# Optimization experiments

Hardware: AMD Instinct MI355X
Metric: run time of the kernel (lower is better)

## Reference

```python
import jax, jax.numpy as jnp
import numpy as np

N_NODES = 100000
N_EDGES = 1600000
IN_C, HID_C, OUT_C = 128, 128, 64


def setup_inputs() -> dict:
    key = jax.random.key(0)
    ks = jax.random.split(key, 8)
    x = jax.random.normal(ks[0], (N_NODES, IN_C), dtype=jnp.float32)
    edge_index = jax.random.randint(ks[1], (2, N_EDGES), 0, N_NODES, dtype=jnp.int64)
    # SAGEConv params: lin_l (aggregated neighbors, with bias), lin_r (root, no bias)
    s1 = 1.0 / np.sqrt(IN_C)
    s2 = 1.0 / np.sqrt(HID_C)
    W1_l = jax.random.uniform(ks[2], (IN_C, HID_C), jnp.float32, -s1, s1)
    b1_l = jnp.zeros((HID_C,), jnp.float32)
    W1_r = jax.random.uniform(ks[3], (IN_C, HID_C), jnp.float32, -s1, s1)
    W2_l = jax.random.uniform(ks[4], (HID_C, OUT_C), jnp.float32, -s2, s2)
    b2_l = jnp.zeros((OUT_C,), jnp.float32)
    W2_r = jax.random.uniform(ks[5], (HID_C, OUT_C), jnp.float32, -s2, s2)
    return {"x": x, "edge_index": edge_index, "W1_l": W1_l, "b1_l": b1_l,
            "W1_r": W1_r, "W2_l": W2_l, "b2_l": b2_l, "W2_r": W2_r}


def _sage_conv(x, src, dst, W_l, b_l, W_r):
    # gather source features, scatter-max reduce onto destinations
    msg = x[src]                                             # [E, C]
    aggr = jax.ops.segment_max(msg, dst, num_segments=N_NODES)
    aggr = jnp.where(jnp.isfinite(aggr), aggr, 0.0)          # isolated nodes -> 0 (PyG behavior)
    return aggr @ W_l + b_l + x @ W_r


def reference(x, edge_index, W1_l, b1_l, W1_r, W2_l, b2_l, W2_r):
    src, dst = edge_index[0], edge_index[1]
    h = _sage_conv(x, src, dst, W1_l, b1_l, W1_r)
    h = jax.nn.relu(h)
    # dropout is identity in eval mode
    out = _sage_conv(h, src, dst, W2_l, b2_l, W2_r)
    return out
```

## Files before the change

### kernel.cpp

```cpp
#include <hip/hip_runtime.h>
#include <cstdint>

#define NNODES 100000
#define NEDGES 1600000
#define NBKT   196
#define CAP    9216
#define BIN_CHUNK 4096
#define GBIN ((NEDGES + BIN_CHUNK - 1) / BIN_CHUNK)
#define GCVT (NNODES * 128 / 8 / 256)

typedef __attribute__((ext_vector_type(8))) __bf16 bf16x8;
typedef __attribute__((ext_vector_type(4))) float f32x4;
typedef short v2s __attribute__((ext_vector_type(2)));

__device__ __forceinline__ unsigned short f2bf_rne(float f) {
    unsigned int u = __float_as_uint(f);
    u += 0x7fffu + ((u >> 16) & 1u);
    return (unsigned short)(u >> 16);
}
__device__ __forceinline__ unsigned encdec(unsigned u) {
    return u ^ (((u & 0x80008000u) >> 15) * 0x7FFFu);
}
__device__ __forceinline__ unsigned pkmax(unsigned a, unsigned b) {
    v2s r = __builtin_elementwise_max(__builtin_bit_cast(v2s, a), __builtin_bit_cast(v2s, b));
    return __builtin_bit_cast(unsigned, r);
}

__global__ __launch_bounds__(256) void prep1_kernel(
        const float* __restrict__ W1l, const float* __restrict__ W1r,
        const float* __restrict__ W2l, const float* __restrict__ W2r,
        uint4* __restrict__ Wf1, uint4* __restrict__ Wf2,
        int* __restrict__ bucketFill) {
    if (blockIdx.x == 24) { bucketFill[threadIdx.x] = 0; return; }
    int t = blockIdx.x * 256 + threadIdx.x;
    unsigned short s[8];
    if (t < 4096) {
        int h = t >> 11, kt = (t >> 9) & 3, nt = (t >> 6) & 7, lane = t & 63;
        const float* W = h ? W1r : W1l;
        int k0 = kt * 32 + (lane >> 4) * 8;
        int col = nt * 16 + (lane & 15);
#pragma unroll
        for (int j = 0; j < 8; ++j) s[j] = f2bf_rne(W[(k0 + j) * 128 + col]);
        uint4 o;
        o.x = (unsigned)s[0] | ((unsigned)s[1] << 16);
        o.y = (unsigned)s[2] | ((unsigned)s[3] << 16);
        o.z = (unsigned)s[4] | ((unsigned)s[5] << 16);
        o.w = (unsigned)s[6] | ((unsigned)s[7] << 16);
        Wf1[t] = o;
    } else {
        int u = t - 4096;
        int h = u >> 10, kt = (u >> 8) & 3, nt = (u >> 6) & 3, lane = u & 63;
        const float* W = h ? W2r : W2l;
        int k0 = kt * 32 + (lane >> 4) * 8;
        int col = nt * 16 + (lane & 15);
#pragma unroll
        for (int j = 0; j < 8; ++j) s[j] = f2bf_rne(W[(k0 + j) * 64 + col]);
        uint4 o;
        o.x = (unsigned)s[0] | ((unsigned)s[1] << 16);
        o.y = (unsigned)s[2] | ((unsigned)s[3] << 16);
        o.z = (unsigned)s[4] | ((unsigned)s[5] << 16);
        o.w = (unsigned)s[6] | ((unsigned)s[7] << 16);
        Wf2[u] = o;
    }
}

__global__ __launch_bounds__(256) void prep2_kernel(
        const int* __restrict__ src, const int* __restrict__ dst,
        unsigned int* __restrict__ binArr, int* __restrict__ bucketFill,
        const float4* __restrict__ xin, uint4* __restrict__ xeout, int nE) {
    if (blockIdx.x >= GBIN) {
        int i = (blockIdx.x - GBIN) * 256 + threadIdx.x;
        float4 v0 = xin[(size_t)2 * i], v1 = xin[(size_t)2 * i + 1];
        uint4 o;
        o.x = encdec((unsigned)f2bf_rne(v0.x) | ((unsigned)f2bf_rne(v0.y) << 16));
        o.y = encdec((unsigned)f2bf_rne(v0.z) | ((unsigned)f2bf_rne(v0.w) << 16));
        o.z = encdec((unsigned)f2bf_rne(v1.x) | ((unsigned)f2bf_rne(v1.y) << 16));
        o.w = encdec((unsigned)f2bf_rne(v1.z) | ((unsigned)f2bf_rne(v1.w) << 16));
        xeout[i] = o;
        return;
    }
    __shared__ unsigned int stage[BIN_CHUNK];
    __shared__ unsigned char bof[BIN_CHUNK];
    __shared__ int cnt[256], cstart[256], cfill[256], gbase[256];
    const int tid = threadIdx.x;
    const int blockStart = blockIdx.x * BIN_CHUNK;
    const int chunkN = min(BIN_CHUNK, nE - blockStart);
    cnt[tid] = 0;
    __syncthreads();
    int myd[16], mys[16];
#pragma unroll
    for (int i = 0; i < 16; ++i) {
        int idx = i * 256 + tid;
        if (idx < chunkN) {
            myd[i] = dst[blockStart + idx];
            mys[i] = src[blockStart + idx];
            atomicAdd(&cnt[myd[i] >> 9], 1);
        }
    }
    __syncthreads();
    int v = cnt[tid];
    for (int off = 1; off < 256; off <<= 1) {
        int add = (tid >= off) ? cnt[tid - off] : 0;
        __syncthreads();
        cnt[tid] += add;
        __syncthreads();
    }
    cstart[tid] = cnt[tid] - v;
    cfill[tid] = cnt[tid] - v;
    if (tid < NBKT && v > 0) gbase[tid] = atomicAdd(&bucketFill[tid], v);
    __syncthreads();
#pragma unroll
    for (int i = 0; i < 16; ++i) {
        int idx = i * 256 + tid;
        if (idx < chunkN) {
            int b = myd[i] >> 9;
            int p = atomicAdd(&cfill[b], 1);
            stage[p] = ((unsigned)(myd[i] & 511) << 17) | (unsigned)mys[i];
            bof[p] = (unsigned char)b;
        }
    }
    __syncthreads();
#pragma unroll
    for (int i = 0; i < 16; ++i) {
        int idx = i * 256 + tid;
        if (idx < chunkN) {
            int b = bof[idx];
            int slot = gbase[b] + (idx - cstart[b]);
            if (slot < CAP) binArr[(size_t)b * CAP + slot] = stage[idx];
        }
    }
}

__global__ __launch_bounds__(512) void build_csr_kernel(
        const unsigned int* __restrict__ binArr, const int* __restrict__ bucketFill,
        unsigned int* __restrict__ sortedSrc,
        int* __restrict__ rowBeg, int* __restrict__ rowEnd) {
    __shared__ unsigned int stage[CAP];
    __shared__ int ncnt[512], nstart[512];
    const int b = blockIdx.x;
    const int t = threadIdx.x;
    const int cnt_b = min(bucketFill[b], CAP);
    ncnt[t] = 0;
    __syncthreads();
    for (int i = t; i < cnt_b; i += 512) {
        unsigned int e = binArr[(size_t)b * CAP + i];
        stage[i] = e;
        atomicAdd(&ncnt[e >> 17], 1);
    }
    __syncthreads();
    int v = ncnt[t];
    for (int off = 1; off < 512; off <<= 1) {
        int add = (t >= off) ? ncnt[t - off] : 0;
        __syncthreads();
        ncnt[t] += add;
        __syncthreads();
    }
    int start = ncnt[t] - v;
    nstart[t] = start;
    int n = (b << 9) + t;
    if (n < NNODES) {
        rowBeg[n] = b * CAP + start;
        rowEnd[n] = b * CAP + start + v;
    }
    __syncthreads();
    for (int i = t; i < cnt_b; i += 512) {
        unsigned int e = stage[i];
        int p = atomicAdd(&nstart[e >> 17], 1);
        sortedSrc[(size_t)b * CAP + p] = e & 0x1FFFFu;
    }
}

__global__ __launch_bounds__(256) void aggregate_pk2(
        const uint4* __restrict__ xe4,
        const int* __restrict__ rowBeg,
        const int* __restrict__ rowEnd,
        const unsigned int* __restrict__ sortedSrc,
        uint4* __restrict__ aggrE,
        int nN) {
    const int wv = threadIdx.x >> 6;
    const int lane = threadIdx.x & 63;
    const int grp = lane >> 4;
    const int nA = blockIdx.x * 8 + wv * 2;
    const int nB = nA + 1;
    if (nA >= nN) return;
    const int begA = rowBeg[nA], endA = rowEnd[nA];
    int begB = 0, endB = 0;
    if (nB < nN) { begB = rowBeg[nB]; endB = rowEnd[nB]; }
    const int mA = endA - begA, mB = endB - begB;

    int idA = (mA > 0) ? (int)sortedSrc[min(begA + lane, endA - 1)] : 0;
    int idB = (mB > 0) ? (int)sortedSrc[min(begB + lane, endB - 1)] : 0;

    unsigned aA0 = 0x80008000u, aA1 = 0x80008000u, aA2 = 0x80008000u, aA3 = 0x80008000u;
    unsigned aB0 = 0x80008000u, aB1 = 0x80008000u, aB2 = 0x80008000u, aB3 = 0x80008000u;

    const int cA = min(mA, 64), cB = min(mB, 64);
    const int mm = max(cA, cB);
    for (int j = 0; j < mm; j += 16) {
        const bool doA = j < cA, doB = j < cB;
        uint4 pA0, pA1, pA2, pA3, pB0, pB1, pB2, pB3;
        if (doA) {
            int s0 = __shfl(idA, j + grp);
            int s1 = __shfl(idA, j + 4 + grp);
            int s2 = __shfl(idA, j + 8 + grp);
            int s3 = __shfl(idA, j + 12 + grp);
            pA0 = xe4[(size_t)s0 * 16 + (lane & 15)];
            pA1 = xe4[(size_t)s1 * 16 + (lane & 15)];
            pA2 = xe4[(size_t)s2 * 16 + (lane & 15)];
            pA3 = xe4[(size_t)s3 * 16 + (lane & 15)];
        }
        if (doB) {
            int s0 = __shfl(idB, j + grp);
            int s1 = __shfl(idB, j + 4 + grp);
            int s2 = __shfl(idB, j + 8 + grp);
            int s3 = __shfl(idB, j + 12 + grp);
            pB0 = xe4[(size_t)s0 * 16 + (lane & 15)];
            pB1 = xe4[(size_t)s1 * 16 + (lane & 15)];
            pB2 = xe4[(size_t)s2 * 16 + (lane & 15)];
            pB3 = xe4[(size_t)s3 * 16 + (lane & 15)];
        }
        if (doA) {
            aA0 = pkmax(aA0, pkmax(pkmax(pA0.x, pA1.x), pkmax(pA2.x, pA3.x)));
            aA1 = pkmax(aA1, pkmax(pkmax(pA0.y, pA1.y), pkmax(pA2.y, pA3.y)));
            aA2 = pkmax(aA2, pkmax(pkmax(pA0.z, pA1.z), pkmax(pA2.z, pA3.z)));
            aA3 = pkmax(aA3, pkmax(pkmax(pA0.w, pA1.w), pkmax(pA2.w, pA3.w)));
        }
        if (doB) {
            aB0 = pkmax(aB0, pkmax(pkmax(pB0.x, pB1.x), pkmax(pB2.x, pB3.x)));
            aB1 = pkmax(aB1, pkmax(pkmax(pB0.y, pB1.y), pkmax(pB2.y, pB3.y)));
            aB2 = pkmax(aB2, pkmax(pkmax(pB0.z, pB1.z), pkmax(pB2.z, pB3.z)));
            aB3 = pkmax(aB3, pkmax(pkmax(pB0.w, pB1.w), pkmax(pB2.w, pB3.w)));
        }
    }
    for (int bs = begA + 64; bs < endA; bs += 64) {
        int bid = (int)sortedSrc[min(bs + lane, endA - 1)];
        const int m = min(endA - bs, 64);
        for (int j = 0; j < m; j += 16) {
            int s0 = __shfl(bid, j + grp);
            int s1 = __shfl(bid, j + 4 + grp);
            int s2 = __shfl(bid, j + 8 + grp);
            int s3 = __shfl(bid, j + 12 + grp);
            uint4 p0 = xe4[(size_t)s0 * 16 + (lane & 15)];
            uint4 p1 = xe4[(size_t)s1 * 16 + (lane & 15)];
            uint4 p2 = xe4[(size_t)s2 * 16 + (lane & 15)];
            uint4 p3 = xe4[(size_t)s3 * 16 + (lane & 15)];
            aA0 = pkmax(aA0, pkmax(pkmax(p0.x, p1.x), pkmax(p2.x, p3.x)));
            aA1 = pkmax(aA1, pkmax(pkmax(p0.y, p1.y), pkmax(p2.y, p3.y)));
            aA2 = pkmax(aA2, pkmax(pkmax(p0.z, p1.z), pkmax(p2.z, p3.z)));
            aA3 = pkmax(aA3, pkmax(pkmax(p0.w, p1.w), pkmax(p2.w, p3.w)));
        }
    }
    for (int bs = begB + 64; bs < endB; bs += 64) {
        int bid = (int)sortedSrc[min(bs + lane, endB - 1)];
        const int m = min(endB - bs, 64);
        for (int j = 0; j < m; j += 16) {
            int s0 = __shfl(bid, j + grp);
            int s1 = __shfl(bid, j + 4 + grp);
            int s2 = __shfl(bid, j + 8 + grp);
            int s3 = __shfl(bid, j + 12 + grp);
            uint4 p0 = xe4[(size_t)s0 * 16 + (lane & 15)];
            uint4 p1 = xe4[(size_t)s1 * 16 + (lane & 15)];
            uint4 p2 = xe4[(size_t)s2 * 16 + (lane & 15)];
            uint4 p3 = xe4[(size_t)s3 * 16 + (lane & 15)];
            aB0 = pkmax(aB0, pkmax(pkmax(p0.x, p1.x), pkmax(p2.x, p3.x)));
            aB1 = pkmax(aB1, pkmax(pkmax(p0.y, p1.y), pkmax(p2.y, p3.y)));
            aB2 = pkmax(aB2, pkmax(pkmax(p0.z, p1.z), pkmax(p2.z, p3.z)));
            aB3 = pkmax(aB3, pkmax(pkmax(p0.w, p1.w), pkmax(p2.w, p3.w)));
        }
    }
    aA0 = pkmax(aA0, (unsigned)__shfl_xor((int)aA0, 16));
    aA1 = pkmax(aA1, (unsigned)__shfl_xor((int)aA1, 16));
    aA2 = pkmax(aA2, (unsigned)__shfl_xor((int)aA2, 16));
    aA3 = pkmax(aA3, (unsigned)__shfl_xor((int)aA3, 16));
    aB0 = pkmax(aB0, (unsigned)__shfl_xor((int)aB0, 16));
    aB1 = pkmax(aB1, (unsigned)__shfl_xor((int)aB1, 16));
    aB2 = pkmax(aB2, (unsigned)__shfl_xor((int)aB2, 16));
    aB3 = pkmax(aB3, (unsigned)__shfl_xor((int)aB3, 16));
    aA0 = pkmax(aA0, (unsigned)__shfl_xor((int)aA0, 32));
    aA1 = pkmax(aA1, (unsigned)__shfl_xor((int)aA1, 32));
    aA2 = pkmax(aA2, (unsigned)__shfl_xor((int)aA2, 32));
    aA3 = pkmax(aA3, (unsigned)__shfl_xor((int)aA3, 32));
    aB0 = pkmax(aB0, (unsigned)__shfl_xor((int)aB0, 32));
    aB1 = pkmax(aB1, (unsigned)__shfl_xor((int)aB1, 32));
    aB2 = pkmax(aB2, (unsigned)__shfl_xor((int)aB2, 32));
    aB3 = pkmax(aB3, (unsigned)__shfl_xor((int)aB3, 32));
    if (lane < 16) {
        uint4 o;
        if (mA > 0) { o.x = aA0; o.y = aA1; o.z = aA2; o.w = aA3; }
        else        { o.x = o.y = o.z = o.w = 0u; }
        aggrE[(size_t)nA * 16 + lane] = o;
    } else if (lane < 32 && nB < nN) {
        uint4 o;
        if (mB > 0) { o.x = aB0; o.y = aB1; o.z = aB2; o.w = aB3; }
        else        { o.x = o.y = o.z = o.w = 0u; }
        aggrE[(size_t)nB * 16 + (lane - 16)] = o;
    }
}

template<int BN, bool RELU, bool ENCOUT, typename OutT>
__global__ __launch_bounds__(256, 4) void sage_gemm_lean(
        const uint4* __restrict__ AggE,
        const uint4* __restrict__ RootE,
        const uint4* __restrict__ Wf,
        const float* __restrict__ bias,
        OutT* __restrict__ C,
        int M) {
    constexpr int NT = BN / 16;
    const int tid = threadIdx.x;
    const int w = tid >> 6;
    const int lane = tid & 63;
    const int quad = lane >> 4;
    const int mrow = lane & 15;
    const int base0 = blockIdx.x * 128 + w * 32;

    const int r0 = min(base0 + mrow, M - 1);
    const int r1 = min(base0 + 16 + mrow, M - 1);

    f32x4 acc[2][NT];
#pragma unroll
    for (int mt = 0; mt < 2; ++mt)
#pragma unroll
        for (int nt = 0; nt < NT; ++nt) acc[mt][nt] = (f32x4){0.f, 0.f, 0.f, 0.f};

#pragma unroll
    for (int kt = 0; kt < 4; ++kt) {
        uint4 ta0 = AggE[(size_t)r0 * 16 + kt * 4 + quad];
        uint4 ta1 = AggE[(size_t)r1 * 16 + kt * 4 + quad];
        uint4 tr0 = RootE[(size_t)r0 * 16 + kt * 4 + quad];
        uint4 tr1 = RootE[(size_t)r1 * 16 + kt * 4 + quad];
        ta0.x = encdec(ta0.x); ta0.y = encdec(ta0.y); ta0.z = encdec(ta0.z); ta0.w = encdec(ta0.w);
        ta1.x = encdec(ta1.x); ta1.y = encdec(ta1.y); ta1.z = encdec(ta1.z); ta1.w = encdec(ta1.w);
        tr0.x = encdec(tr0.x); tr0.y = encdec(tr0.y); tr0.z = encdec(tr0.z); tr0.w = encdec(tr0.w);
        tr1.x = encdec(tr1.x); tr1.y = encdec(tr1.y); tr1.z = encdec(tr1.z); tr1.w = encdec(tr1.w);
        bf16x8 aa0 = __builtin_bit_cast(bf16x8, ta0);
        bf16x8 aa1 = __builtin_bit_cast(bf16x8, ta1);
        bf16x8 ar0 = __builtin_bit_cast(bf16x8, tr0);
        bf16x8 ar1 = __builtin_bit_cast(bf16x8, tr1);
#pragma unroll
        for (int nt = 0; nt < NT; ++nt) {
            bf16x8 b0 = __builtin_bit_cast(bf16x8, Wf[(kt * NT + nt) * 64 + lane]);
            acc[0][nt] = __builtin_amdgcn_mfma_f32_16x16x32_bf16(aa0, b0, acc[0][nt], 0, 0, 0);
            acc[1][nt] = __builtin_amdgcn_mfma_f32_16x16x32_bf16(aa1, b0, acc[1][nt], 0, 0, 0);
            bf16x8 b1 = __builtin_bit_cast(bf16x8, Wf[((4 + kt) * NT + nt) * 64 + lane]);
            acc[0][nt] = __builtin_amdgcn_mfma_f32_16x16x32_bf16(ar0, b1, acc[0][nt], 0, 0, 0);
            acc[1][nt] = __builtin_amdgcn_mfma_f32_16x16x32_bf16(ar1, b1, acc[1][nt], 0, 0, 0);
        }
    }

#pragma unroll
    for (int mt = 0; mt < 2; ++mt) {
        const int rowD = base0 + mt * 16 + quad * 4;
#pragma unroll
        for (int nt = 0; nt < NT; ++nt) {
            int col = nt * 16 + mrow;
            float bv = bias[col];
#pragma unroll
            for (int r = 0; r < 4; ++r) {
                int grow = rowD + r;
                if (grow < M) {
                    float v = acc[mt][nt][r] + bv;
                    if (RELU) v = fmaxf(v, 0.0f);
                    if constexpr (ENCOUT) {
                        unsigned u = f2bf_rne(v);
                        u ^= ((u >> 15) & 1u) * 0x7FFFu;
                        C[(size_t)grow * BN + col] = (OutT)u;
                    } else {
                        C[(size_t)grow * BN + col] = (OutT)v;
                    }
                }
            }
        }
    }
}

extern "C" void kernel_launch(void* const* d_in, const int* in_sizes, int n_in,
                              void* d_out, int out_size, void* d_ws, size_t ws_size,
                              hipStream_t stream) {
    const float* x   = (const float*)d_in[0];
    const int*   ei  = (const int*)d_in[1];
    const float* W1l = (const float*)d_in[2];
    const float* b1l = (const float*)d_in[3];
    const float* W1r = (const float*)d_in[4];
    const float* W2l = (const float*)d_in[5];
    const float* b2l = (const float*)d_in[6];
    const float* W2r = (const float*)d_in[7];
    float* out = (float*)d_out;

    const int* src = ei;
    const int* dst = ei + NEDGES;

    char* ws = (char*)d_ws;
    unsigned short* xe    = (unsigned short*)ws; ws += (size_t)NNODES * 128 * 2;
    unsigned short* he    = (unsigned short*)ws; ws += (size_t)NNODES * 128 * 2;
    unsigned short* aggrE = (unsigned short*)ws; ws += (size_t)NNODES * 128 * 2;
    unsigned int* binArr    = (unsigned int*)ws; ws += (size_t)NBKT * CAP * 4;
    unsigned int* sortedSrc = (unsigned int*)ws; ws += (size_t)NBKT * CAP * 4;
    int* rowBeg     = (int*)ws; ws += (size_t)NNODES * 4;
    int* rowEnd     = (int*)ws; ws += (size_t)NNODES * 4;
    int* bucketFill = (int*)ws; ws += 256 * 4;
    uint4* Wf1 = (uint4*)ws; ws += 4096 * 16;
    uint4* Wf2 = (uint4*)ws; ws += 2048 * 16;

    const int gAgg = (NNODES + 7) / 8;
    const int gGemm = (NNODES + 127) / 128;

    prep1_kernel<<<25, 256, 0, stream>>>(W1l, W1r, W2l, W2r, Wf1, Wf2, bucketFill);
    prep2_kernel<<<GBIN + GCVT, 256, 0, stream>>>(src, dst, binArr, bucketFill,
                                                  (const float4*)x, (uint4*)xe, NEDGES);
    build_csr_kernel<<<NBKT, 512, 0, stream>>>(binArr, bucketFill, sortedSrc, rowBeg, rowEnd);

    aggregate_pk2<<<gAgg, 256, 0, stream>>>((const uint4*)xe, rowBeg, rowEnd, sortedSrc,
                                            (uint4*)aggrE, NNODES);
    sage_gemm_lean<128, true, true, unsigned short><<<gGemm, 256, 0, stream>>>(
        (const uint4*)aggrE, (const uint4*)xe, Wf1, b1l, he, NNODES);
    aggregate_pk2<<<gAgg, 256, 0, stream>>>((const uint4*)he, rowBeg, rowEnd, sortedSrc,
                                            (uint4*)aggrE, NNODES);
    sage_gemm_lean<64, false, false, float><<<gGemm, 256, 0, stream>>>(
        (const uint4*)aggrE, (const uint4*)he, Wf2, b2l, out, NNODES);
}
```

Before: 294.8 us.

## Pipeline aggregation across node pairs by prefetching next CSR rows and neighbor ids

The aggregation kernel now has each wavefront process 8 destination nodes in 4 pairs instead of one pair. It prefetches the next pair's row bounds and neighbor-id list while the current pair's feature gathers are in flight, hiding the dependent index-load latency. The first 16 neighbors are gathered unconditionally, which relies on every node having at least one edge or on out-of-range ids being clamped safely, and the grid assumes NNODES divides by 32. Launch bounds are raised to 4 blocks per CU.

```diff
diff --git a/kernel.cpp b/kernel.cpp
--- a/kernel.cpp
+++ b/kernel.cpp
@@ -170,130 +170,166 @@
     }
 }
 
-__global__ __launch_bounds__(256) void aggregate_pk2(
+__global__ __launch_bounds__(256, 4) void aggregate_pipe(
         const uint4* __restrict__ xe4,
         const int* __restrict__ rowBeg,
         const int* __restrict__ rowEnd,
         const unsigned int* __restrict__ sortedSrc,
-        uint4* __restrict__ aggrE,
-        int nN) {
-    const int wv = threadIdx.x >> 6;
+        uint4* __restrict__ aggrE) {
     const int lane = threadIdx.x & 63;
     const int grp = lane >> 4;
-    const int nA = blockIdx.x * 8 + wv * 2;
-    const int nB = nA + 1;
-    if (nA >= nN) return;
-    const int begA = rowBeg[nA], endA = rowEnd[nA];
-    int begB = 0, endB = 0;
-    if (nB < nN) { begB = rowBeg[nB]; endB = rowEnd[nB]; }
-    const int mA = endA - begA, mB = endB - begB;
-
-    int idA = (mA > 0) ? (int)sortedSrc[min(begA + lane, endA - 1)] : 0;
-    int idB = (mB > 0) ? (int)sortedSrc[min(begB + lane, endB - 1)] : 0;
-
-    unsigned aA0 = 0x80008000u, aA1 = 0x80008000u, aA2 = 0x80008000u, aA3 = 0x80008000u;
-    unsigned aB0 = 0x80008000u, aB1 = 0x80008000u, aB2 = 0x80008000u, aB3 = 0x80008000u;
-
-    const int cA = min(mA, 64), cB = min(mB, 64);
-    const int mm = max(cA, cB);
-    for (int j = 0; j < mm; j += 16) {
-        const bool doA = j < cA, doB = j < cB;
-        uint4 pA0, pA1, pA2, pA3, pB0, pB1, pB2, pB3;
-        if (doA) {
-            int s0 = __shfl(idA, j + grp);
-            int s1 = __shfl(idA, j + 4 + grp);
-            int s2 = __shfl(idA, j + 8 + grp);
-            int s3 = __shfl(idA, j + 12 + grp);
-            pA0 = xe4[(size_t)s0 * 16 + (lane & 15)];
-            pA1 = xe4[(size_t)s1 * 16 + (lane & 15)];
-            pA2 = xe4[(size_t)s2 * 16 + (lane & 15)];
-            pA3 = xe4[(size_t)s3 * 16 + (lane & 15)];
-        }
-        if (doB) {
-            int s0 = __shfl(idB, j + grp);
-            int s1 = __shfl(idB, j + 4 + grp);
-            int s2 = __shfl(idB, j + 8 + grp);
-            int s3 = __shfl(idB, j + 12 + grp);
-            pB0 = xe4[(size_t)s0 * 16 + (lane & 15)];
-            pB1 = xe4[(size_t)s1 * 16 + (lane & 15)];
-            pB2 = xe4[(size_t)s2 * 16 + (lane & 15)];
-            pB3 = xe4[(size_t)s3 * 16 + (lane & 15)];
-        }
-        if (doA) {
-            aA0 = pkmax(aA0, pkmax(pkmax(pA0.x, pA1.x), pkmax(pA2.x, pA3.x)));
-            aA1 = pkmax(aA1, pkmax(pkmax(pA0.y, pA1.y), pkmax(pA2.y, pA3.y)));
-            aA2 = pkmax(aA2, pkmax(pkmax(pA0.z, pA1.z), pkmax(pA2.z, pA3.z)));
-            aA3 = pkmax(aA3, pkmax(pkmax(pA0.w, pA1.w), pkmax(pA2.w, pA3.w)));
-        }
-        if (doB) {
-            aB0 = pkmax(aB0, pkmax(pkmax(pB0.x, pB1.x), pkmax(pB2.x, pB3.x)));
-            aB1 = pkmax(aB1, pkmax(pkmax(pB0.y, pB1.y), pkmax(pB2.y, pB3.y)));
-            aB2 = pkmax(aB2, pkmax(pkmax(pB0.z, pB1.z), pkmax(pB2.z, pB3.z)));
-            aB3 = pkmax(aB3, pkmax(pkmax(pB0.w, pB1.w), pkmax(pB2.w, pB3.w)));
-        }
-    }
-    for (int bs = begA + 64; bs < endA; bs += 64) {
-        int bid = (int)sortedSrc[min(bs + lane, endA - 1)];
-        const int m = min(endA - bs, 64);
-        for (int j = 0; j < m; j += 16) {
-            int s0 = __shfl(bid, j + grp);
-            int s1 = __shfl(bid, j + 4 + grp);
-            int s2 = __shfl(bid, j + 8 + grp);
-            int s3 = __shfl(bid, j + 12 + grp);
-            uint4 p0 = xe4[(size_t)s0 * 16 + (lane & 15)];
-            uint4 p1 = xe4[(size_t)s1 * 16 + (lane & 15)];
-            uint4 p2 = xe4[(size_t)s2 * 16 + (lane & 15)];
-            uint4 p3 = xe4[(size_t)s3 * 16 + (lane & 15)];
-            aA0 = pkmax(aA0, pkmax(pkmax(p0.x, p1.x), pkmax(p2.x, p3.x)));
-            aA1 = pkmax(aA1, pkmax(pkmax(p0.y, p1.y), pkmax(p2.y, p3.y)));
-            aA2 = pkmax(aA2, pkmax(pkmax(p0.z, p1.z), pkmax(p2.z, p3.z)));
-            aA3 = pkmax(aA3, pkmax(pkmax(p0.w, p1.w), pkmax(p2.w, p3.w)));
-        }
-    }
-    for (int bs = begB + 64; bs < endB; bs += 64) {
-        int bid = (int)sortedSrc[min(bs + lane, endB - 1)];
-        const int m = min(endB - bs, 64);
-        for (int j = 0; j < m; j += 16) {
-            int s0 = __shfl(bid, j + grp);
-            int s1 = __shfl(bid, j + 4 + grp);
-            int s2 = __shfl(bid, j + 8 + grp);
-            int s3 = __shfl(bid, j + 12 + grp);
-            uint4 p0 = xe4[(size_t)s0 * 16 + (lane & 15)];
-            uint4 p1 = xe4[(size_t)s1 * 16 + (lane & 15)];
-            uint4 p2 = xe4[(size_t)s2 * 16 + (lane & 15)];
-            uint4 p3 = xe4[(size_t)s3 * 16 + (lane & 15)];
-            aB0 = pkmax(aB0, pkmax(pkmax(p0.x, p1.x), pkmax(p2.x, p3.x)));
-            aB1 = pkmax(aB1, pkmax(pkmax(p0.y, p1.y), pkmax(p2.y, p3.y)));
-            aB2 = pkmax(aB2, pkmax(pkmax(p0.z, p1.z), pkmax(p2.z, p3.z)));
-            aB3 = pkmax(aB3, pkmax(pkmax(p0.w, p1.w), pkmax(p2.w, p3.w)));
-        }
-    }
-    aA0 = pkmax(aA0, (unsigned)__shfl_xor((int)aA0, 16));
-    aA1 = pkmax(aA1, (unsigned)__shfl_xor((int)aA1, 16));
-    aA2 = pkmax(aA2, (unsigned)__shfl_xor((int)aA2, 16));
-    aA3 = pkmax(aA3, (unsigned)__shfl_xor((int)aA3, 16));
-    aB0 = pkmax(aB0, (unsigned)__shfl_xor((int)aB0, 16));
-    aB1 = pkmax(aB1, (unsigned)__shfl_xor((int)aB1, 16));
-    aB2 = pkmax(aB2, (unsigned)__shfl_xor((int)aB2, 16));
-    aB3 = pkmax(aB3, (unsigned)__shfl_xor((int)aB3, 16));
-    aA0 = pkmax(aA0, (unsigned)__shfl_xor((int)aA0, 32));
-    aA1 = pkmax(aA1, (unsigned)__shfl_xor((int)aA1, 32));
-    aA2 = pkmax(aA2, (unsigned)__shfl_xor((int)aA2, 32));
-    aA3 = pkmax(aA3, (unsigned)__shfl_xor((int)aA3, 32));
-    aB0 = pkmax(aB0, (unsigned)__shfl_xor((int)aB0, 32));
-    aB1 = pkmax(aB1, (unsigned)__shfl_xor((int)aB1, 32));
-    aB2 = pkmax(aB2, (unsigned)__shfl_xor((int)aB2, 32));
-    aB3 = pkmax(aB3, (unsigned)__shfl_xor((int)aB3, 32));
-    if (lane < 16) {
-        uint4 o;
-        if (mA > 0) { o.x = aA0; o.y = aA1; o.z = aA2; o.w = aA3; }
-        else        { o.x = o.y = o.z = o.w = 0u; }
-        aggrE[(size_t)nA * 16 + lane] = o;
-    } else if (lane < 32 && nB < nN) {
-        uint4 o;
-        if (mB > 0) { o.x = aB0; o.y = aB1; o.z = aB2; o.w = aB3; }
-        else        { o.x = o.y = o.z = o.w = 0u; }
-        aggrE[(size_t)nB * 16 + (lane - 16)] = o;
+    const int col = lane & 15;
+    const int base = blockIdx.x * 32 + (threadIdx.x >> 6) * 8;
+
+    int begA = rowBeg[base + 0], endA = rowEnd[base + 0];
+    int begB = rowBeg[base + 1], endB = rowEnd[base + 1];
+    int idA = (endA > begA) ? (int)sortedSrc[min(begA + lane, endA - 1)] : 0;
+    int idB = (endB > begB) ? (int)sortedSrc[min(begB + lane, endB - 1)] : 0;
+
+    for (int p = 0; p < 4; ++p) {
+        const int nA = base + 2 * p, nB = nA + 1;
+        const int mA = endA - begA, mB = endB - begB;
+
+        int begA2 = 0, endA2 = 0, begB2 = 0, endB2 = 0;
+        if (p < 3) {
+            begA2 = rowBeg[nA + 2]; endA2 = rowEnd[nA + 2];
+            begB2 = rowBeg[nB + 2]; endB2 = rowEnd[nB + 2];
+        }
+
+        int sA0 = __shfl(idA, grp),     sA1 = __shfl(idA, 4 + grp);
+        int sA2 = __shfl(idA, 8 + grp), sA3 = __shfl(idA, 12 + grp);
+        int sB0 = __shfl(idB, grp),     sB1 = __shfl(idB, 4 + grp);
+        int sB2 = __shfl(idB, 8 + grp), sB3 = __shfl(idB, 12 + grp);
+        uint4 pA0 = xe4[(size_t)sA0 * 16 + col];
+        uint4 pA1 = xe4[(size_t)sA1 * 16 + col];
+        uint4 pA2 = xe4[(size_t)sA2 * 16 + col];
+        uint4 pA3 = xe4[(size_t)sA3 * 16 + col];
+        uint4 pB0 = xe4[(size_t)sB0 * 16 + col];
+        uint4 pB1 = xe4[(size_t)sB1 * 16 + col];
+        uint4 pB2 = xe4[(size_t)sB2 * 16 + col];
+        uint4 pB3 = xe4[(size_t)sB3 * 16 + col];
+
+        int idA2 = 0, idB2 = 0;
+        if (p < 3) {
+            idA2 = (endA2 > begA2) ? (int)sortedSrc[min(begA2 + lane, endA2 - 1)] : 0;
+            idB2 = (endB2 > begB2) ? (int)sortedSrc[min(begB2 + lane, endB2 - 1)] : 0;
+        }
+
+        unsigned aA0 = pkmax(pkmax(pA0.x, pA1.x), pkmax(pA2.x, pA3.x));
+        unsigned aA1 = pkmax(pkmax(pA0.y, pA1.y), pkmax(pA2.y, pA3.y));
+        unsigned aA2 = pkmax(pkmax(pA0.z, pA1.z), pkmax(pA2.z, pA3.z));
+        unsigned aA3 = pkmax(pkmax(pA0.w, pA1.w), pkmax(pA2.w, pA3.w));
+        unsigned aB0 = pkmax(pkmax(pB0.x, pB1.x), pkmax(pB2.x, pB3.x));
+        unsigned aB1 = pkmax(pkmax(pB0.y, pB1.y), pkmax(pB2.y, pB3.y));
+        unsigned aB2 = pkmax(pkmax(pB0.z, pB1.z), pkmax(pB2.z, pB3.z));
+        unsigned aB3 = pkmax(pkmax(pB0.w, pB1.w), pkmax(pB2.w, pB3.w));
+
+        const int cA = min(mA, 64), cB = min(mB, 64);
+        const int mm = max(cA, cB);
+        for (int j = 16; j < mm; j += 16) {
+            const bool doA = j < cA, doB = j < cB;
+            uint4 qA0, qA1, qA2, qA3, qB0, qB1, qB2, qB3;
+            if (doA) {
+                int s0 = __shfl(idA, j + grp);
+                int s1 = __shfl(idA, j + 4 + grp);
+                int s2 = __shfl(idA, j + 8 + grp);
+                int s3 = __shfl(idA, j + 12 + grp);
+                qA0 = xe4[(size_t)s0 * 16 + col];
+                qA1 = xe4[(size_t)s1 * 16 + col];
+                qA2 = xe4[(size_t)s2 * 16 + col];
+                qA3 = xe4[(size_t)s3 * 16 + col];
+            }
+            if (doB) {
+                int s0 = __shfl(idB, j + grp);
+                int s1 = __shfl(idB, j + 4 + grp);
+                int s2 = __shfl(idB, j + 8 + grp);
+                int s3 = __shfl(idB, j + 12 + grp);
+                qB0 = xe4[(size_t)s0 * 16 + col];
+                qB1 = xe4[(size_t)s1 * 16 + col];
+                qB2 = xe4[(size_t)s2 * 16 + col];
+                qB3 = xe4[(size_t)s3 * 16 + col];
+            }
+            if (doA) {
+                aA0 = pkmax(aA0, pkmax(pkmax(qA0.x, qA1.x), pkmax(qA2.x, qA3.x)));
+                aA1 = pkmax(aA1, pkmax(pkmax(qA0.y, qA1.y), pkmax(qA2.y, qA3.y)));
+                aA2 = pkmax(aA2, pkmax(pkmax(qA0.z, qA1.z), pkmax(qA2.z, qA3.z)));
+                aA3 = pkmax(aA3, pkmax(pkmax(qA0.w, qA1.w), pkmax(qA2.w, qA3.w)));
+            }
+            if (doB) {
+                aB0 = pkmax(aB0, pkmax(pkmax(qB0.x, qB1.x), pkmax(qB2.x, qB3.x)));
+                aB1 = pkmax(aB1, pkmax(pkmax(qB0.y, qB1.y), pkmax(qB2.y, qB3.y)));
+                aB2 = pkmax(aB2, pkmax(pkmax(qB0.z, qB1.z), pkmax(qB2.z, qB3.z)));
+                aB3 = pkmax(aB3, pkmax(pkmax(qB0.w, qB1.w), pkmax(qB2.w, qB3.w)));
+            }
+        }
+        for (int bs = begA + 64; bs < endA; bs += 64) {
+            int bid = (int)sortedSrc[min(bs + lane, endA - 1)];
+            const int m = min(endA - bs, 64);
+            for (int j = 0; j < m; j += 16) {
+                int s0 = __shfl(bid, j + grp);
+                int s1 = __shfl(bid, j + 4 + grp);
+                int s2 = __shfl(bid, j + 8 + grp);
+                int s3 = __shfl(bid, j + 12 + grp);
+                uint4 q0 = xe4[(size_t)s0 * 16 + col];
+                uint4 q1 = xe4[(size_t)s1 * 16 + col];
+                uint4 q2 = xe4[(size_t)s2 * 16 + col];
+                uint4 q3 = xe4[(size_t)s3 * 16 + col];
+                aA0 = pkmax(aA0, pkmax(pkmax(q0.x, q1.x), pkmax(q2.x, q3.x)));
+                aA1 = pkmax(aA1, pkmax(pkmax(q0.y, q1.y), pkmax(q2.y, q3.y)));
+                aA2 = pkmax(aA2, pkmax(pkmax(q0.z, q1.z), pkmax(q2.z, q3.z)));
+                aA3 = pkmax(aA3, pkmax(pkmax(q0.w, q1.w), pkmax(q2.w, q3.w)));
+            }
+        }
+        for (int bs = begB + 64; bs < endB; bs += 64) {
+            int bid = (int)sortedSrc[min(bs + lane, endB - 1)];
+            const int m = min(endB - bs, 64);
+            for (int j = 0; j < m; j += 16) {
+                int s0 = __shfl(bid, j + grp);
+                int s1 = __shfl(bid, j + 4 + grp);
+                int s2 = __shfl(bid, j + 8 + grp);
+                int s3 = __shfl(bid, j + 12 + grp);
+                uint4 q0 = xe4[(size_t)s0 * 16 + col];
+                uint4 q1 = xe4[(size_t)s1 * 16 + col];
+                uint4 q2 = xe4[(size_t)s2 * 16 + col];
+                uint4 q3 = xe4[(size_t)s3 * 16 + col];
+                aB0 = pkmax(aB0, pkmax(pkmax(q0.x, q1.x), pkmax(q2.x, q3.x)));
+                aB1 = pkmax(aB1, pkmax(pkmax(q0.y, q1.y), pkmax(q2.y, q3.y)));
+                aB2 = pkmax(aB2, pkmax(pkmax(q0.z, q1.z), pkmax(q2.z, q3.z)));
+                aB3 = pkmax(aB3, pkmax(pkmax(q0.w, q1.w), pkmax(q2.w, q3.w)));
+            }
+        }
+
+        aA0 = pkmax(aA0, (unsigned)__shfl_xor((int)aA0, 16));
+        aA1 = pkmax(aA1, (unsigned)__shfl_xor((int)aA1, 16));
+        aA2 = pkmax(aA2, (unsigned)__shfl_xor((int)aA2, 16));
+        aA3 = pkmax(aA3, (unsigned)__shfl_xor((int)aA3, 16));
+        aB0 = pkmax(aB0, (unsigned)__shfl_xor((int)aB0, 16));
+        aB1 = pkmax(aB1, (unsigned)__shfl_xor((int)aB1, 16));
+        aB2 = pkmax(aB2, (unsigned)__shfl_xor((int)aB2, 16));
+        aB3 = pkmax(aB3, (unsigned)__shfl_xor((int)aB3, 16));
+        aA0 = pkmax(aA0, (unsigned)__shfl_xor((int)aA0, 32));
+        aA1 = pkmax(aA1, (unsigned)__shfl_xor((int)aA1, 32));
+        aA2 = pkmax(aA2, (unsigned)__shfl_xor((int)aA2, 32));
+        aA3 = pkmax(aA3, (unsigned)__shfl_xor((int)aA3, 32));
+        aB0 = pkmax(aB0, (unsigned)__shfl_xor((int)aB0, 32));
+        aB1 = pkmax(aB1, (unsigned)__shfl_xor((int)aB1, 32));
+        aB2 = pkmax(aB2, (unsigned)__shfl_xor((int)aB2, 32));
+        aB3 = pkmax(aB3, (unsigned)__shfl_xor((int)aB3, 32));
+
+        if (lane < 16) {
+            uint4 o;
+            if (mA > 0) { o.x = aA0; o.y = aA1; o.z = aA2; o.w = aA3; }
+            else        { o.x = o.y = o.z = o.w = 0u; }
+            aggrE[(size_t)nA * 16 + lane] = o;
+        } else if (lane < 32) {
+            uint4 o;
+            if (mB > 0) { o.x = aB0; o.y = aB1; o.z = aB2; o.w = aB3; }
+            else        { o.x = o.y = o.z = o.w = 0u; }
+            aggrE[(size_t)nB * 16 + (lane - 16)] = o;
+        }
+
+        begA = begA2; endA = endA2; begB = begB2; endB = endB2;
+        idA = idA2; idB = idB2;
     }
 }
 
@@ -401,7 +437,7 @@
     uint4* Wf1 = (uint4*)ws; ws += 4096 * 16;
     uint4* Wf2 = (uint4*)ws; ws += 2048 * 16;
 
-    const int gAgg = (NNODES + 7) / 8;
+    const int gAgg = NNODES / 32;
     const int gGemm = (NNODES + 127) / 128;
 
     prep1_kernel<<<25, 256, 0, stream>>>(W1l, W1r, W2l, W2r, Wf1, Wf2, bucketFill);
@@ -409,12 +445,12 @@
                                                   (const float4*)x, (uint4*)xe, NEDGES);
     build_csr_kernel<<<NBKT, 512, 0, stream>>>(binArr, bucketFill, sortedSrc, rowBeg, rowEnd);
 
-    aggregate_pk2<<<gAgg, 256, 0, stream>>>((const uint4*)xe, rowBeg, rowEnd, sortedSrc,
-                                            (uint4*)aggrE, NNODES);
+    aggregate_pipe<<<gAgg, 256, 0, stream>>>((const uint4*)xe, rowBeg, rowEnd, sortedSrc,
+                                             (uint4*)aggrE);
     sage_gemm_lean<128, true, true, unsigned short><<<gGemm, 256, 0, stream>>>(
         (const uint4*)aggrE, (const uint4*)xe, Wf1, b1l, he, NNODES);
-    aggregate_pk2<<<gAgg, 256, 0, stream>>>((const uint4*)he, rowBeg, rowEnd, sortedSrc,
-                                            (uint4*)aggrE, NNODES);
+    aggregate_pipe<<<gAgg, 256, 0, stream>>>((const uint4*)he, rowBeg, rowEnd, sortedSrc,
+                                             (uint4*)aggrE);
     sage_gemm_lean<64, false, false, float><<<gGemm, 256, 0, stream>>>(
         (const uint4*)aggrE, (const uint4*)he, Wf2, b2l, out, NNODES);
 }
```

New measurement: 299.9 us. About the same (+1.7%).

## Slice node features into 8 channel slabs for cache-local gather aggregation

Applied to the files above, without the earlier changes.

Stores bf16 node features in eight 32-byte channel slices (slice-major) instead of row-major 256-byte rows. The aggregation kernel now assigns each block to one slice and 32 nodes, so each gather touches only a 3.2 MB slab that can stay resident in cache. The GEMM input loads and the layer-1 output store are rewritten to use the sliced layout. In exchange, every gather fetches only 32 bytes, the edge indices are re-read once per slice, and threads in a wave loop to the highest degree among their 8 nodes.

```diff
diff --git a/kernel.cpp b/kernel.cpp
--- a/kernel.cpp
+++ b/kernel.cpp
@@ -25,6 +25,13 @@
     v2s r = __builtin_elementwise_max(__builtin_bit_cast(v2s, a), __builtin_bit_cast(v2s, b));
     return __builtin_bit_cast(unsigned, r);
 }
+__device__ __forceinline__ uint4 pkmax4(uint4 a, uint4 b) {
+    uint4 r;
+    r.x = pkmax(a.x, b.x); r.y = pkmax(a.y, b.y);
+    r.z = pkmax(a.z, b.z); r.w = pkmax(a.w, b.w);
+    return r;
+}
+
 
 __global__ __launch_bounds__(256) void prep1_kernel(
         const float* __restrict__ W1l, const float* __restrict__ W1r,
@@ -69,14 +76,18 @@
         unsigned int* __restrict__ binArr, int* __restrict__ bucketFill,
         const float4* __restrict__ xin, uint4* __restrict__ xeout, int nE) {
     if (blockIdx.x >= GBIN) {
-        int i = (blockIdx.x - GBIN) * 256 + threadIdx.x;
-        float4 v0 = xin[(size_t)2 * i], v1 = xin[(size_t)2 * i + 1];
+        int t = (blockIdx.x - GBIN) * 256 + threadIdx.x;
+        int s = t / (NNODES * 2);
+        int rem = t - s * (NNODES * 2);
+        int n = rem >> 1, hh = rem & 1;
+        int f = n * 32 + s * 4 + hh * 2;
+        float4 v0 = xin[f], v1 = xin[f + 1];
         uint4 o;
         o.x = encdec((unsigned)f2bf_rne(v0.x) | ((unsigned)f2bf_rne(v0.y) << 16));
         o.y = encdec((unsigned)f2bf_rne(v0.z) | ((unsigned)f2bf_rne(v0.w) << 16));
         o.z = encdec((unsigned)f2bf_rne(v1.x) | ((unsigned)f2bf_rne(v1.y) << 16));
         o.w = encdec((unsigned)f2bf_rne(v1.z) | ((unsigned)f2bf_rne(v1.w) << 16));
-        xeout[i] = o;
+        xeout[t] = o;
         return;
     }
     __shared__ unsigned int stage[BIN_CHUNK];
@@ -170,130 +181,64 @@
     }
 }
 
-__global__ __launch_bounds__(256) void aggregate_pk2(
-        const uint4* __restrict__ xe4,
+__global__ __launch_bounds__(256) void aggregate_sl(
+        const uint4* __restrict__ xsl,
         const int* __restrict__ rowBeg,
         const int* __restrict__ rowEnd,
         const unsigned int* __restrict__ sortedSrc,
-        uint4* __restrict__ aggrE,
+        uint4* __restrict__ asl,
         int nN) {
-    const int wv = threadIdx.x >> 6;
+    const int s    = blockIdx.x & 7;
+    const int g    = blockIdx.x >> 3;
+    const int wv   = threadIdx.x >> 6;
     const int lane = threadIdx.x & 63;
-    const int grp = lane >> 4;
-    const int nA = blockIdx.x * 8 + wv * 2;
-    const int nB = nA + 1;
-    if (nA >= nN) return;
-    const int begA = rowBeg[nA], endA = rowEnd[nA];
-    int begB = 0, endB = 0;
-    if (nB < nN) { begB = rowBeg[nB]; endB = rowEnd[nB]; }
-    const int mA = endA - begA, mB = endB - begB;
-
-    int idA = (mA > 0) ? (int)sortedSrc[min(begA + lane, endA - 1)] : 0;
-    int idB = (mB > 0) ? (int)sortedSrc[min(begB + lane, endB - 1)] : 0;
-
-    unsigned aA0 = 0x80008000u, aA1 = 0x80008000u, aA2 = 0x80008000u, aA3 = 0x80008000u;
-    unsigned aB0 = 0x80008000u, aB1 = 0x80008000u, aB2 = 0x80008000u, aB3 = 0x80008000u;
-
-    const int cA = min(mA, 64), cB = min(mB, 64);
-    const int mm = max(cA, cB);
-    for (int j = 0; j < mm; j += 16) {
-        const bool doA = j < cA, doB = j < cB;
-        uint4 pA0, pA1, pA2, pA3, pB0, pB1, pB2, pB3;
-        if (doA) {
-            int s0 = __shfl(idA, j + grp);
-            int s1 = __shfl(idA, j + 4 + grp);
-            int s2 = __shfl(idA, j + 8 + grp);
-            int s3 = __shfl(idA, j + 12 + grp);
-            pA0 = xe4[(size_t)s0 * 16 + (lane & 15)];
-            pA1 = xe4[(size_t)s1 * 16 + (lane & 15)];
-            pA2 = xe4[(size_t)s2 * 16 + (lane & 15)];
-            pA3 = xe4[(size_t)s3 * 16 + (lane & 15)];
-        }
-        if (doB) {
-            int s0 = __shfl(idB, j + grp);
-            int s1 = __shfl(idB, j + 4 + grp);
-            int s2 = __shfl(idB, j + 8 + grp);
-            int s3 = __shfl(idB, j + 12 + grp);
-            pB0 = xe4[(size_t)s0 * 16 + (lane & 15)];
-            pB1 = xe4[(size_t)s1 * 16 + (lane & 15)];
-            pB2 = xe4[(size_t)s2 * 16 + (lane & 15)];
-            pB3 = xe4[(size_t)s3 * 16 + (lane & 15)];
-        }
-        if (doA) {
-            aA0 = pkmax(aA0, pkmax(pkmax(pA0.x, pA1.x), pkmax(pA2.x, pA3.x)));
-            aA1 = pkmax(aA1, pkmax(pkmax(pA0.y, pA1.y), pkmax(pA2.y, pA3.y)));
-            aA2 = pkmax(aA2, pkmax(pkmax(pA0.z, pA1.z), pkmax(pA2.z, pA3.z)));
-            aA3 = pkmax(aA3, pkmax(pkmax(pA0.w, pA1.w), pkmax(pA2.w, pA3.w)));
-        }
-        if (doB) {
-            aB0 = pkmax(aB0, pkmax(pkmax(pB0.x, pB1.x), pkmax(pB2.x, pB3.x)));
-            aB1 = pkmax(aB1, pkmax(pkmax(pB0.y, pB1.y), pkmax(pB2.y, pB3.y)));
-            aB2 = pkmax(aB2, pkmax(pkmax(pB0.z, pB1.z), pkmax(pB2.z, pB3.z)));
-            aB3 = pkmax(aB3, pkmax(pkmax(pB0.w, pB1.w), pkmax(pB2.w, pB3.w)));
-        }
-    }
-    for (int bs = begA + 64; bs < endA; bs += 64) {
-        int bid = (int)sortedSrc[min(bs + lane, endA - 1)];
-        const int m = min(endA - bs, 64);
-        for (int j = 0; j < m; j += 16) {
-            int s0 = __shfl(bid, j + grp);
-            int s1 = __shfl(bid, j + 4 + grp);
-            int s2 = __shfl(bid, j + 8 + grp);
-            int s3 = __shfl(bid, j + 12 + grp);
-            uint4 p0 = xe4[(size_t)s0 * 16 + (lane & 15)];
-            uint4 p1 = xe4[(size_t)s1 * 16 + (lane & 15)];
-            uint4 p2 = xe4[(size_t)s2 * 16 + (lane & 15)];
-            uint4 p3 = xe4[(size_t)s3 * 16 + (lane & 15)];
-            aA0 = pkmax(aA0, pkmax(pkmax(p0.x, p1.x), pkmax(p2.x, p3.x)));
-            aA1 = pkmax(aA1, pkmax(pkmax(p0.y, p1.y), pkmax(p2.y, p3.y)));
-            aA2 = pkmax(aA2, pkmax(pkmax(p0.z, p1.z), pkmax(p2.z, p3.z)));
-            aA3 = pkmax(aA3, pkmax(pkmax(p0.w, p1.w), pkmax(p2.w, p3.w)));
-        }
-    }
-    for (int bs = begB + 64; bs < endB; bs += 64) {
-        int bid = (int)sortedSrc[min(bs + lane, endB - 1)];
-        const int m = min(endB - bs, 64);
-        for (int j = 0; j < m; j += 16) {
-            int s0 = __shfl(bid, j + grp);
-            int s1 = __shfl(bid, j + 4 + grp);
-            int s2 = __shfl(bid, j + 8 + grp);
-            int s3 = __shfl(bid, j + 12 + grp);
-            uint4 p0 = xe4[(size_t)s0 * 16 + (lane & 15)];
-            uint4 p1 = xe4[(size_t)s1 * 16 + (lane & 15)];
-            uint4 p2 = xe4[(size_t)s2 * 16 + (lane & 15)];
-            uint4 p3 = xe4[(size_t)s3 * 16 + (lane & 15)];
-            aB0 = pkmax(aB0, pkmax(pkmax(p0.x, p1.x), pkmax(p2.x, p3.x)));
-            aB1 = pkmax(aB1, pkmax(pkmax(p0.y, p1.y), pkmax(p2.y, p3.y)));
-            aB2 = pkmax(aB2, pkmax(pkmax(p0.z, p1.z), pkmax(p2.z, p3.z)));
-            aB3 = pkmax(aB3, pkmax(pkmax(p0.w, p1.w), pkmax(p2.w, p3.w)));
-        }
-    }
-    aA0 = pkmax(aA0, (unsigned)__shfl_xor((int)aA0, 16));
-    aA1 = pkmax(aA1, (unsigned)__shfl_xor((int)aA1, 16));
-    aA2 = pkmax(aA2, (unsigned)__shfl_xor((int)aA2, 16));
-    aA3 = pkmax(aA3, (unsigned)__shfl_xor((int)aA3, 16));
-    aB0 = pkmax(aB0, (unsigned)__shfl_xor((int)aB0, 16));
-    aB1 = pkmax(aB1, (unsigned)__shfl_xor((int)aB1, 16));
-    aB2 = pkmax(aB2, (unsigned)__shfl_xor((int)aB2, 16));
-    aB3 = pkmax(aB3, (unsigned)__shfl_xor((int)aB3, 16));
-    aA0 = pkmax(aA0, (unsigned)__shfl_xor((int)aA0, 32));
-    aA1 = pkmax(aA1, (unsigned)__shfl_xor((int)aA1, 32));
-    aA2 = pkmax(aA2, (unsigned)__shfl_xor((int)aA2, 32));
-    aA3 = pkmax(aA3, (unsigned)__shfl_xor((int)aA3, 32));
-    aB0 = pkmax(aB0, (unsigned)__shfl_xor((int)aB0, 32));
-    aB1 = pkmax(aB1, (unsigned)__shfl_xor((int)aB1, 32));
-    aB2 = pkmax(aB2, (unsigned)__shfl_xor((int)aB2, 32));
-    aB3 = pkmax(aB3, (unsigned)__shfl_xor((int)aB3, 32));
-    if (lane < 16) {
+    const int k    = lane >> 3;
+    const int sub  = (lane >> 1) & 3;
+    const int h    = lane & 1;
+    const int n    = g * 32 + wv * 8 + k;
+    const size_t sbase = (size_t)s * nN;
+
+    const int beg = rowBeg[n], end = rowEnd[n];
+    const int m = end - beg;
+
+    int maxm = m;
+    maxm = max(maxm, __shfl_xor(maxm, 8));
+    maxm = max(maxm, __shfl_xor(maxm, 16));
+    maxm = max(maxm, __shfl_xor(maxm, 32));
+
+    int id0 = 0, id1 = 0, id2 = 0, id3 = 0;
+    if (m > 0) {
+        id0 = (int)sortedSrc[min(beg + sub,      end - 1)];
+        id1 = (int)sortedSrc[min(beg + 4 + sub,  end - 1)];
+        id2 = (int)sortedSrc[min(beg + 8 + sub,  end - 1)];
+        id3 = (int)sortedSrc[min(beg + 12 + sub, end - 1)];
+    }
+    uint4 p0 = xsl[(sbase + id0) * 2 + h];
+    uint4 p1 = xsl[(sbase + id1) * 2 + h];
+    uint4 p2 = xsl[(sbase + id2) * 2 + h];
+    uint4 p3 = xsl[(sbase + id3) * 2 + h];
+    uint4 acc = pkmax4(pkmax4(p0, p1), pkmax4(p2, p3));
+
+    for (int e0 = 16; e0 < maxm; e0 += 4) {
+        int idt = (m > 0) ? (int)sortedSrc[min(beg + e0 + sub, end - 1)] : 0;
+        uint4 q = xsl[(sbase + idt) * 2 + h];
+        acc = pkmax4(acc, q);
+    }
+
+    acc.x = pkmax(acc.x, (unsigned)__shfl_xor((int)acc.x, 2));
+    acc.y = pkmax(acc.y, (unsigned)__shfl_xor((int)acc.y, 2));
+    acc.z = pkmax(acc.z, (unsigned)__shfl_xor((int)acc.z, 2));
+    acc.w = pkmax(acc.w, (unsigned)__shfl_xor((int)acc.w, 2));
+    acc.x = pkmax(acc.x, (unsigned)__shfl_xor((int)acc.x, 4));
+    acc.y = pkmax(acc.y, (unsigned)__shfl_xor((int)acc.y, 4));
+    acc.z = pkmax(acc.z, (unsigned)__shfl_xor((int)acc.z, 4));
+    acc.w = pkmax(acc.w, (unsigned)__shfl_xor((int)acc.w, 4));
+
+    const unsigned ok = (m > 0) ? 0xFFFFFFFFu : 0u;
+    if (sub == 0) {
         uint4 o;
-        if (mA > 0) { o.x = aA0; o.y = aA1; o.z = aA2; o.w = aA3; }
-        else        { o.x = o.y = o.z = o.w = 0u; }
-        aggrE[(size_t)nA * 16 + lane] = o;
-    } else if (lane < 32 && nB < nN) {
-        uint4 o;
-        if (mB > 0) { o.x = aB0; o.y = aB1; o.z = aB2; o.w = aB3; }
-        else        { o.x = o.y = o.z = o.w = 0u; }
-        aggrE[(size_t)nB * 16 + (lane - 16)] = o;
+        o.x = acc.x & ok; o.y = acc.y & ok; o.z = acc.z & ok; o.w = acc.w & ok;
+        asl[(sbase + n) * 2 + h] = o;
     }
 }
 
@@ -324,10 +269,12 @@
 
 #pragma unroll
     for (int kt = 0; kt < 4; ++kt) {
-        uint4 ta0 = AggE[(size_t)r0 * 16 + kt * 4 + quad];
-        uint4 ta1 = AggE[(size_t)r1 * 16 + kt * 4 + quad];
-        uint4 tr0 = RootE[(size_t)r0 * 16 + kt * 4 + quad];
-        uint4 tr1 = RootE[(size_t)r1 * 16 + kt * 4 + quad];
+        const int q = kt * 4 + quad;
+        const size_t sl = ((size_t)(q >> 1) * M) * 2 + (q & 1);
+        uint4 ta0 = AggE[sl + (size_t)r0 * 2];
+        uint4 ta1 = AggE[sl + (size_t)r1 * 2];
+        uint4 tr0 = RootE[sl + (size_t)r0 * 2];
+        uint4 tr1 = RootE[sl + (size_t)r1 * 2];
         ta0.x = encdec(ta0.x); ta0.y = encdec(ta0.y); ta0.z = encdec(ta0.z); ta0.w = encdec(ta0.w);
         ta1.x = encdec(ta1.x); ta1.y = encdec(ta1.y); ta1.z = encdec(ta1.z); ta1.w = encdec(ta1.w);
         tr0.x = encdec(tr0.x); tr0.y = encdec(tr0.y); tr0.z = encdec(tr0.z); tr0.w = encdec(tr0.w);
@@ -363,7 +310,7 @@
                     if constexpr (ENCOUT) {
                         unsigned u = f2bf_rne(v);
                         u ^= ((u >> 15) & 1u) * 0x7FFFu;
-                        C[(size_t)grow * BN + col] = (OutT)u;
+                        C[((size_t)nt * M + grow) * 16 + mrow] = (OutT)u;
                     } else {
                         C[(size_t)grow * BN + col] = (OutT)v;
                     }
@@ -401,7 +348,7 @@
     uint4* Wf1 = (uint4*)ws; ws += 4096 * 16;
     uint4* Wf2 = (uint4*)ws; ws += 2048 * 16;
 
-    const int gAgg = (NNODES + 7) / 8;
+    const int gAgg = (NNODES / 32) * 8;
     const int gGemm = (NNODES + 127) / 128;
 
     prep1_kernel<<<25, 256, 0, stream>>>(W1l, W1r, W2l, W2r, Wf1, Wf2, bucketFill);
@@ -409,12 +356,12 @@
                                                   (const float4*)x, (uint4*)xe, NEDGES);
     build_csr_kernel<<<NBKT, 512, 0, stream>>>(binArr, bucketFill, sortedSrc, rowBeg, rowEnd);
 
-    aggregate_pk2<<<gAgg, 256, 0, stream>>>((const uint4*)xe, rowBeg, rowEnd, sortedSrc,
-                                            (uint4*)aggrE, NNODES);
+    aggregate_sl<<<gAgg, 256, 0, stream>>>((const uint4*)xe, rowBeg, rowEnd, sortedSrc,
+                                           (uint4*)aggrE, NNODES);
     sage_gemm_lean<128, true, true, unsigned short><<<gGemm, 256, 0, stream>>>(
         (const uint4*)aggrE, (const uint4*)xe, Wf1, b1l, he, NNODES);
-    aggregate_pk2<<<gAgg, 256, 0, stream>>>((const uint4*)he, rowBeg, rowEnd, sortedSrc,
-                                            (uint4*)aggrE, NNODES);
+    aggregate_sl<<<gAgg, 256, 0, stream>>>((const uint4*)he, rowBeg, rowEnd, sortedSrc,
+                                           (uint4*)aggrE, NNODES);
     sage_gemm_lean<64, false, false, float><<<gGemm, 256, 0, stream>>>(
         (const uint4*)aggrE, (const uint4*)he, Wf2, b2l, out, NNODES);
 }
```

New measurement: 322.3 us. 9.3% more time.
